# Kernel optimization log

Hardware: AMD Instinct MI355X
Metric: run time of the kernel (lower is better)

## Reference

```python
import jax, jax.numpy as jnp
import numpy as np

# Model dims
D_MODEL = 768
N_LAYER = 2
VOCAB = 32000
D_STATE = 16
D_INNER = 2 * D_MODEL          # expand=2
DT_RANK = D_MODEL // 16        # 48
D_CONV = 4
EPS = 1e-5


def rmsnorm(x, w):
    return x * jax.lax.rsqrt(jnp.mean(x * x, axis=-1, keepdims=True) + EPS) * w


def selective_scan(u, delta, A, B, C, D):
    # u: (b,l,di) delta: (b,l,di) A: (di,n) B,C: (b,l,n) D: (di,)
    def step(h, inp):
        delta_t, B_t, C_t, u_t = inp  # (b,di),(b,n),(b,n),(b,di)
        dA = jnp.exp(delta_t[..., None] * A)                      # (b,di,n)
        dBu = delta_t[..., None] * B_t[:, None, :] * u_t[..., None]
        h = dA * h + dBu
        y = jnp.einsum('bdn,bn->bd', h, C_t)
        return h, y

    b = u.shape[0]
    h0 = jnp.zeros((b, D_INNER, D_STATE), dtype=u.dtype)
    xs = (jnp.swapaxes(delta, 0, 1), jnp.swapaxes(B, 0, 1),
          jnp.swapaxes(C, 0, 1), jnp.swapaxes(u, 0, 1))
    _, ys = jax.lax.scan(step, h0, xs)        # ys: (l,b,di)
    y = jnp.swapaxes(ys, 0, 1)
    return y + u * D


def mamba_block(x, in_proj_w, conv_w, conv_b, x_proj_w, dt_proj_w, dt_proj_b,
                A_log, D, out_proj_w):
    b, l, d = x.shape
    xr = x @ in_proj_w.T                       # (b,l,2*di)
    u, res = jnp.split(xr, 2, axis=-1)
    # causal depthwise conv over seq
    uc = jnp.swapaxes(u, 1, 2)                 # (b,di,l)
    uc = jax.lax.conv_general_dilated(
        uc, conv_w[:, None, :], window_strides=(1,),
        padding=[(D_CONV - 1, 0)], feature_group_count=D_INNER,
        dimension_numbers=('NCH', 'OIH', 'NCH'))
    u = jax.nn.silu(jnp.swapaxes(uc + conv_b[None, :, None], 1, 2))
    # ssm
    A = -jnp.exp(A_log)                        # (di,n)
    x_dbl = u @ x_proj_w.T                     # (b,l,dt_rank+2n)
    delta, B, C = jnp.split(x_dbl, [DT_RANK, DT_RANK + D_STATE], axis=-1)
    delta = jax.nn.softplus(delta @ dt_proj_w.T + dt_proj_b)   # (b,l,di)
    y = selective_scan(u, delta, A, B, C, D)
    y = y * jax.nn.silu(res)
    return y @ out_proj_w.T


def setup_inputs() -> dict:
    key = jax.random.key(0)
    ks = jax.random.split(key, 12)
    s = 0.02
    L = N_LAYER
    inp = {
        'input_ids': jax.random.randint(ks[0], (2, 1024), 0, VOCAB),
        'emb': jax.random.normal(ks[1], (VOCAB, D_MODEL), jnp.float32) * s,
        'norm_w': jnp.ones((L, D_MODEL), jnp.float32),
        'in_proj_w': jax.random.normal(ks[2], (L, 2 * D_INNER, D_MODEL), jnp.float32) * s,
        'conv_w': jax.random.normal(ks[3], (L, D_INNER, D_CONV), jnp.float32) * s,
        'conv_b': jnp.zeros((L, D_INNER), jnp.float32),
        'x_proj_w': jax.random.normal(ks[4], (L, DT_RANK + 2 * D_STATE, D_INNER), jnp.float32) * s,
        'dt_proj_w': jax.random.normal(ks[5], (L, D_INNER, DT_RANK), jnp.float32) * s,
        'dt_proj_b': jax.random.normal(ks[6], (L, D_INNER), jnp.float32) * s,
        'A_log': jnp.log(jnp.broadcast_to(jnp.arange(1, D_STATE + 1, dtype=jnp.float32),
                                          (L, D_INNER, D_STATE))),
        'D': jnp.ones((L, D_INNER), jnp.float32),
        'out_proj_w': jax.random.normal(ks[7], (L, D_MODEL, D_INNER), jnp.float32) * s,
        'norm_f_w': jnp.ones((D_MODEL,), jnp.float32),
    }
    return inp


def reference(input_ids, emb, norm_w, in_proj_w, conv_w, conv_b, x_proj_w,
              dt_proj_w, dt_proj_b, A_log, D, out_proj_w, norm_f_w):
    x = emb[input_ids]                         # (b,l,d)
    for i in range(N_LAYER):
        x = x + mamba_block(rmsnorm(x, norm_w[i]), in_proj_w[i], conv_w[i],
                            conv_b[i], x_proj_w[i], dt_proj_w[i], dt_proj_b[i],
                            A_log[i], D[i], out_proj_w[i])
    x = rmsnorm(x, norm_f_w)
    logits = x @ emb.T                         # tied lm_head
    return logits
```

## Files before the change

kernel.cpp:

```cpp
#include <hip/hip_runtime.h>
#include <hip/hip_bf16.h>
#include <cstdint>
#include <cstddef>

#define D_MODEL 768
#define D_INNER 1536
#define DT_RANK 48
#define D_STATE 16
#define SEQ     1024
#define BATCH   2
#define NROWS   2048
#define VOCAB   32000
#define LCHUNK  16
#define NCHUNK  64
#define CHST    49152

typedef __hip_bfloat16 bf16;
typedef short bf16x8 __attribute__((ext_vector_type(8)));
typedef float f32x4  __attribute__((ext_vector_type(4)));
struct bf8 { bf16 v[8]; };

__device__ __forceinline__ void async_copy16(void* lds, const void* gp) {
    __builtin_amdgcn_global_load_lds(
        (const __attribute__((address_space(1))) unsigned int*)gp,
        (__attribute__((address_space(3)))       unsigned int*)lds,
        16, 0, 0);
}

template<int EPI>
__global__ __launch_bounds__(256) void gemm_bt(
    const bf16* __restrict__ A, const bf16* __restrict__ B,
    float* __restrict__ C, const float* __restrict__ bias,
    int M, int N, int K, int ntm)
{
    __shared__ bf16 sA[128 * 32];
    __shared__ bf16 sB[128 * 32];
    const int bid  = blockIdx.x;
    const int m0   = (bid % ntm) * 128;
    const int n0   = (bid / ntm) * 128;
    const int t    = threadIdx.x;
    const int wave = t >> 6;
    const int lane = t & 63;
    const int r0 = wave * 16 + (lane >> 2);
    const int c0 = (lane & 3) * 8;
    const int wm = (wave & 1) * 64;
    const int wn = (wave >> 1) * 64;
    const int fm = lane & 15;
    const int kq = (lane >> 4) * 8;

    f32x4 acc[4][4];
    #pragma unroll
    for (int i = 0; i < 4; ++i)
        #pragma unroll
        for (int j = 0; j < 4; ++j)
            acc[i][j] = {0.f, 0.f, 0.f, 0.f};

    int nr0 = n0 + r0;      if (nr0 > N - 1) nr0 = N - 1;
    int nr1 = n0 + 64 + r0; if (nr1 > N - 1) nr1 = N - 1;

    const bf16* gA0 = A + (size_t)(m0 + r0)      * K + c0;
    const bf16* gA1 = A + (size_t)(m0 + 64 + r0) * K + c0;
    const bf16* gB0 = B + (size_t)nr0 * K + c0;
    const bf16* gB1 = B + (size_t)nr1 * K + c0;
    char* lA0 = (char*)sA + wave * 1024;
    char* lA1 = (char*)sA + 4096 + wave * 1024;
    char* lB0 = (char*)sB + wave * 1024;
    char* lB1 = (char*)sB + 4096 + wave * 1024;

    for (int k0 = 0; k0 < K; k0 += 32) {
        async_copy16(lA0, gA0 + k0);
        async_copy16(lA1, gA1 + k0);
        async_copy16(lB0, gB0 + k0);
        async_copy16(lB1, gB1 + k0);
        __syncthreads();

        bf16x8 af[4], bfr[4];
        #pragma unroll
        for (int i = 0; i < 4; ++i) {
            af[i]  = *(const bf16x8*)&sA[(wm + i * 16 + fm) * 32 + kq];
            bfr[i] = *(const bf16x8*)&sB[(wn + i * 16 + fm) * 32 + kq];
        }
        #pragma unroll
        for (int i = 0; i < 4; ++i)
            #pragma unroll
            for (int j = 0; j < 4; ++j)
                acc[i][j] = __builtin_amdgcn_mfma_f32_16x16x32_bf16(
                    af[i], bfr[j], acc[i][j], 0, 0, 0);
        __syncthreads();
    }

    const int lr = (lane >> 4) * 4;
    const int lc = lane & 15;
    #pragma unroll
    for (int i = 0; i < 4; ++i) {
        #pragma unroll
        for (int j = 0; j < 4; ++j) {
            const int col = n0 + wn + j * 16 + lc;
            if (col >= N) continue;
            #pragma unroll
            for (int r = 0; r < 4; ++r) {
                const int row = m0 + wm + i * 16 + lr + r;
                const size_t o = (size_t)row * N + col;
                float v = acc[i][j][r];
                if (EPI == 1) {
                    C[o] += v;
                } else if (EPI == 2) {
                    v += bias[col];
                    v = (v > 15.f) ? v : __logf(1.f + __expf(v));
                    C[o] = v;
                } else {
                    C[o] = v;
                }
            }
        }
    }
}

__global__ __launch_bounds__(192) void embed_kernel(
    const int* __restrict__ ids, const float* __restrict__ emb,
    float* __restrict__ x)
{
    const int row = blockIdx.x;
    const int t = threadIdx.x;
    const float4* src = (const float4*)(emb + (size_t)ids[row] * D_MODEL);
    float4* dst = (float4*)(x + (size_t)row * D_MODEL);
    dst[t] = src[t];
}

__global__ __launch_bounds__(256) void rmsnorm_kernel(
    const float* __restrict__ x, const float* __restrict__ w,
    bf16* __restrict__ out)
{
    const int row = blockIdx.x;
    const float* xr = x + (size_t)row * D_MODEL;
    const int t = threadIdx.x;
    float v0 = xr[t], v1 = xr[t + 256], v2 = xr[t + 512];
    float s = v0 * v0 + v1 * v1 + v2 * v2;
    #pragma unroll
    for (int m = 1; m < 64; m <<= 1) s += __shfl_xor(s, m);
    __shared__ float red[4];
    if ((t & 63) == 0) red[t >> 6] = s;
    __syncthreads();
    s = red[0] + red[1] + red[2] + red[3];
    const float sc = rsqrtf(s * (1.f / 768.f) + 1e-5f);
    bf16* o = out + (size_t)row * D_MODEL;
    o[t]       = __float2bfloat16(v0 * sc * w[t]);
    o[t + 256] = __float2bfloat16(v1 * sc * w[t + 256]);
    o[t + 512] = __float2bfloat16(v2 * sc * w[t + 512]);
}

__global__ __launch_bounds__(256) void cvt_bf16_kernel(
    const float* __restrict__ src, bf16* __restrict__ dst, int n)
{
    const int i = (blockIdx.x * 256 + threadIdx.x) * 8;
    if (i >= n) return;
    const float4 a = *(const float4*)(src + i);
    const float4 b = *(const float4*)(src + i + 4);
    bf8 o;
    o.v[0] = __float2bfloat16(a.x); o.v[1] = __float2bfloat16(a.y);
    o.v[2] = __float2bfloat16(a.z); o.v[3] = __float2bfloat16(a.w);
    o.v[4] = __float2bfloat16(b.x); o.v[5] = __float2bfloat16(b.y);
    o.v[6] = __float2bfloat16(b.z); o.v[7] = __float2bfloat16(b.w);
    *(bf8*)(dst + i) = o;
}

__global__ __launch_bounds__(256) void cvt_layer_weights(
    const float* __restrict__ ipw, const float* __restrict__ xpw,
    const float* __restrict__ dtw, const float* __restrict__ opw,
    bf16* __restrict__ wip, bf16* __restrict__ wxp,
    bf16* __restrict__ wdt, bf16* __restrict__ wop)
{
    int i = blockIdx.x * 256 + threadIdx.x;
    if (i < 3072 * 768) { wip[i] = __float2bfloat16(ipw[i]); return; }
    i -= 3072 * 768;
    if (i < 80 * 1536)  { wxp[i] = __float2bfloat16(xpw[i]); return; }
    i -= 80 * 1536;
    if (i < 1536 * 64) {
        const int r = i >> 6, c = i & 63;
        wdt[i] = __float2bfloat16(c < DT_RANK ? dtw[r * DT_RANK + c] : 0.f);
        return;
    }
    i -= 1536 * 64;
    if (i < 768 * 1536) { wop[i] = __float2bfloat16(opw[i]); }
}

__global__ __launch_bounds__(256) void pad_dt_kernel(
    const float* __restrict__ x_dbl, bf16* __restrict__ out)
{
    const int i = blockIdx.x * 256 + threadIdx.x;
    const int r = i >> 6, c = i & 63;
    out[i] = __float2bfloat16(c < DT_RANK ? x_dbl[r * 80 + c] : 0.f);
}

__global__ __launch_bounds__(256) void conv_silu_kernel(
    const float* __restrict__ xr, const float* __restrict__ cw,
    const float* __restrict__ cb, float* __restrict__ uf,
    bf16* __restrict__ ub)
{
    const int idx = blockIdx.x * 256 + threadIdx.x;
    const int di  = idx % D_INNER;
    const int row = idx / D_INNER;
    const int l   = row & (SEQ - 1);
    float acc = cb[di];
    #pragma unroll
    for (int j = 0; j < 4; ++j) {
        const int ll = l - 3 + j;
        if (ll >= 0)
            acc += cw[di * 4 + j] * xr[(size_t)(row - 3 + j) * 3072 + di];
    }
    const float s = acc / (1.f + __expf(-acc));
    uf[idx] = s;
    ub[idx] = __float2bfloat16(s);
}

__global__ __launch_bounds__(256) void scan_pass1(
    const float* __restrict__ delta, const float* __restrict__ u,
    const float* __restrict__ x_dbl, const float* __restrict__ A_log,
    float* __restrict__ P, float* __restrict__ H)
{
    const int n  = threadIdx.x & 15;
    const int g  = threadIdx.x >> 4;
    const int ch = blockIdx.x * 16 + g;
    const int k  = blockIdx.y;
    const int b  = ch / D_INNER;
    const int di = ch % D_INNER;
    const int t0 = k * LCHUNK;

    const float An = -__expf(A_log[di * D_STATE + n]);
    const float* drow = delta + ((size_t)b * SEQ + t0) * D_INNER + di;
    const float* urow = u     + ((size_t)b * SEQ + t0) * D_INNER + di;
    const float* xdr  = x_dbl + ((size_t)b * SEQ + t0) * 80;

    float h = 0.f, ap = 1.f;
    #pragma unroll
    for (int t = 0; t < LCHUNK; ++t) {
        const float dv = drow[t * D_INNER];
        const float uv = urow[t * D_INNER];
        const float Bv = xdr[t * 80 + 48 + n];
        const float a  = __expf(dv * An);
        h = a * h + (dv * Bv) * uv;
        ap *= a;
    }
    const size_t o = (size_t)k * CHST + ch * 16 + n;
    P[o] = ap;
    H[o] = h;
}

__global__ __launch_bounds__(256) void scan_pass2(
    const float* __restrict__ P, const float* __restrict__ H,
    float* __restrict__ Hin)
{
    const int id = blockIdx.x * 256 + threadIdx.x;
    float h = 0.f;
    #pragma unroll 16
    for (int k = 0; k < NCHUNK; ++k) {
        const size_t o = (size_t)k * CHST + id;
        Hin[o] = h;
        h = P[o] * h + H[o];
    }
}

__global__ __launch_bounds__(256) void scan_pass3(
    const float* __restrict__ delta, const float* __restrict__ u,
    const float* __restrict__ x_dbl, const float* __restrict__ xr,
    const float* __restrict__ A_log, const float* __restrict__ Dp,
    const float* __restrict__ Hin, bf16* __restrict__ yb)
{
    const int n  = threadIdx.x & 15;
    const int g  = threadIdx.x >> 4;
    const int ch = blockIdx.x * 16 + g;
    const int k  = blockIdx.y;
    const int b  = ch / D_INNER;
    const int di = ch % D_INNER;
    const int t0 = k * LCHUNK;

    const float An = -__expf(A_log[di * D_STATE + n]);
    const float Dv = Dp[di];
    const float* drow = delta + ((size_t)b * SEQ + t0) * D_INNER + di;
    const float* urow = u     + ((size_t)b * SEQ + t0) * D_INNER + di;
    const float* rrow = xr + ((size_t)b * SEQ + t0) * 3072 + D_INNER + di;
    const float* xdr  = x_dbl + ((size_t)b * SEQ + t0) * 80;
    bf16* yrow = yb + ((size_t)b * SEQ + t0) * D_INNER + di;

    float h = Hin[(size_t)k * CHST + ch * 16 + n];
    #pragma unroll
    for (int t = 0; t < LCHUNK; ++t) {
        const float dv = drow[t * D_INNER];
        const float uv = urow[t * D_INNER];
        const float Bv = xdr[t * 80 + 48 + n];
        const float Cv = xdr[t * 80 + 64 + n];
        const float a  = __expf(dv * An);
        h = a * h + (dv * Bv) * uv;
        float p = h * Cv;
        p += __shfl_xor(p, 1);
        p += __shfl_xor(p, 2);
        p += __shfl_xor(p, 4);
        p += __shfl_xor(p, 8);
        if (n == 0) {
            float y = p + uv * Dv;
            const float r = rrow[t * 3072];
            y *= r / (1.f + __expf(-r));
            yrow[t * D_INNER] = __float2bfloat16(y);
        }
    }
}

extern "C" void kernel_launch(void* const* d_in, const int* in_sizes, int n_in,
                              void* d_out, int out_size, void* d_ws, size_t ws_size,
                              hipStream_t stream)
{
    const int*   ids    = (const int*)  d_in[0];
    const float* emb    = (const float*)d_in[1];
    const float* norm_w = (const float*)d_in[2];
    const float* ipw    = (const float*)d_in[3];
    const float* cw     = (const float*)d_in[4];
    const float* cb     = (const float*)d_in[5];
    const float* xpw    = (const float*)d_in[6];
    const float* dtw    = (const float*)d_in[7];
    const float* dtb    = (const float*)d_in[8];
    const float* alog   = (const float*)d_in[9];
    const float* Dp     = (const float*)d_in[10];
    const float* opw    = (const float*)d_in[11];
    const float* nfw    = (const float*)d_in[12];
    float* out = (float*)d_out;

    char* ws = (char*)d_ws;
    bf16*  emb_bf = (bf16*)ws;  ws += (size_t)VOCAB * D_MODEL * 2;
    float* x      = (float*)ws; ws += (size_t)NROWS * D_MODEL * 4;
    bf16*  xn     = (bf16*)ws;  ws += (size_t)NROWS * D_MODEL * 2;
    bf16*  ub     = (bf16*)ws;  ws += (size_t)NROWS * D_INNER * 2;
    float* xdbl   = (float*)ws; ws += (size_t)NROWS * 80 * 4;
    bf16*  dtraw  = (bf16*)ws;  ws += (size_t)NROWS * 64 * 2;
    bf16*  yb     = (bf16*)ws;  ws += (size_t)NROWS * D_INNER * 2;
    bf16*  wip    = (bf16*)ws;  ws += (size_t)3072 * 768 * 2;
    bf16*  wxp    = (bf16*)ws;  ws += (size_t)80 * 1536 * 2;
    bf16*  wdt    = (bf16*)ws;  ws += (size_t)1536 * 64 * 2;
    bf16*  wop    = (bf16*)ws;  ws += (size_t)768 * 1536 * 2;

    char* ob = (char*)d_out;
    float* xr    = (float*)ob;  ob += (size_t)NROWS * 3072 * 4;
    float* uf    = (float*)ob;  ob += (size_t)NROWS * D_INNER * 4;
    float* delta = (float*)ob;  ob += (size_t)NROWS * D_INNER * 4;
    float* Pbuf  = (float*)ob;  ob += (size_t)NCHUNK * CHST * 4;
    float* Hbuf  = (float*)ob;  ob += (size_t)NCHUNK * CHST * 4;
    float* Hin   = (float*)ob;  ob += (size_t)NCHUNK * CHST * 4;

    cvt_bf16_kernel<<<VOCAB * D_MODEL / 8 / 256, 256, 0, stream>>>(
        emb, emb_bf, VOCAB * D_MODEL);
    embed_kernel<<<NROWS, 192, 0, stream>>>(ids, emb, x);

    for (int l = 0; l < 2; ++l) {
        cvt_layer_weights<<<(3760128 + 255) / 256, 256, 0, stream>>>(
            ipw + (size_t)l * 3072 * 768, xpw + (size_t)l * 80 * 1536,
            dtw + (size_t)l * 1536 * DT_RANK, opw + (size_t)l * 768 * 1536,
            wip, wxp, wdt, wop);
        rmsnorm_kernel<<<NROWS, 256, 0, stream>>>(x, norm_w + l * D_MODEL, xn);
        gemm_bt<0><<<16 * 24, 256, 0, stream>>>(xn, wip, xr, nullptr,
                                                NROWS, 3072, D_MODEL, 16);
        conv_silu_kernel<<<NROWS * D_INNER / 256, 256, 0, stream>>>(
            xr, cw + (size_t)l * D_INNER * 4, cb + (size_t)l * D_INNER, uf, ub);
        gemm_bt<0><<<16 * 1, 256, 0, stream>>>(ub, wxp, xdbl, nullptr,
                                               NROWS, 80, D_INNER, 16);
        pad_dt_kernel<<<NROWS * 64 / 256, 256, 0, stream>>>(xdbl, dtraw);
        gemm_bt<2><<<16 * 12, 256, 0, stream>>>(dtraw, wdt, delta,
                                                dtb + (size_t)l * D_INNER,
                                                NROWS, D_INNER, 64, 16);
        scan_pass1<<<dim3(192, NCHUNK), 256, 0, stream>>>(
            delta, uf, xdbl, alog + (size_t)l * D_INNER * D_STATE, Pbuf, Hbuf);
        scan_pass2<<<CHST / 256, 256, 0, stream>>>(Pbuf, Hbuf, Hin);
        scan_pass3<<<dim3(192, NCHUNK), 256, 0, stream>>>(
            delta, uf, xdbl, xr, alog + (size_t)l * D_INNER * D_STATE,
            Dp + (size_t)l * D_INNER, Hin, yb);
        gemm_bt<1><<<16 * 6, 256, 0, stream>>>(yb, wop, x, nullptr,
                                               NROWS, D_MODEL, D_INNER, 16);
    }

    rmsnorm_kernel<<<NROWS, 256, 0, stream>>>(x, nfw, xn);
    gemm_bt<0><<<16 * 250, 256, 0, stream>>>(xn, emb_bf, out, nullptr,
                                             NROWS, VOCAB, D_MODEL, 16);
}
```

Measured before the change: 1.054 ms.

## Add 256x256 pipelined GEMM for lm_head and split-K the x_proj GEMM

Adds a 512-thread GEMM kernel with 256x256 tiles, 64-wide K steps, double-buffered swizzled LDS staging via async global-to-LDS loads, interleaved MFMA phases and an XCD-aware block remap. It is used for the large tied lm_head projection (2048x32000x768), which dominates runtime. The tiny x_proj GEMM, previously launched on only 16 blocks, is split along K into 4 partial products and then reduced by a new kernel to raise parallelism. The new kernel uses 128KB of LDS and relies on the dimensions dividing 256 exactly, with no bounds checks.

```diff
diff --git a/kernel.cpp b/kernel.cpp
--- a/kernel.cpp
+++ b/kernel.cpp
@@ -27,17 +27,165 @@
         16, 0, 0);
 }
 
+
+#define LDSP(BUF, AB) (smem + (((BUF)*2 + (AB)) << 15))
+
+#define PHB() do { \
+  __builtin_amdgcn_sched_barrier(0); \
+  __builtin_amdgcn_s_barrier(); \
+  __builtin_amdgcn_sched_barrier(0); \
+} while (0)
+
+#define WAIT_VMCNT(n) do { \
+  asm volatile("s_waitcnt vmcnt(" #n ")" ::: "memory"); \
+  __builtin_amdgcn_sched_barrier(0); \
+} while (0)
+
+#define STAGE_A(BUF, H, KT) do { \
+  const int ru0_ = (H)*64 + wave*8; \
+  const int ru1_ = ru0_ + 128; \
+  const bf16* ga0_ = Ag + (size_t)(m0 + ru0_ + (lane >> 3)) * (size_t)K + (size_t)((KT)*64 + swz8); \
+  const bf16* ga1_ = Ag + (size_t)(m0 + ru1_ + (lane >> 3)) * (size_t)K + (size_t)((KT)*64 + swz8); \
+  async_copy16(LDSP(BUF, 0) + ru0_*128, ga0_); \
+  async_copy16(LDSP(BUF, 0) + ru1_*128, ga1_); \
+} while (0)
+
+#define STAGE_B(BUF, H, KT) do { \
+  const int lb0_ = wave*8, lb1_ = 64 + wave*8; \
+  const int rb0_ = ((lb0_ >> 5) << 6) + (H)*32 + (lb0_ & 31); \
+  const int rb1_ = ((lb1_ >> 5) << 6) + (H)*32 + (lb1_ & 31); \
+  const bf16* gb0_ = Bg + (size_t)(n0 + rb0_ + (lane >> 3)) * (size_t)K + (size_t)((KT)*64 + swz8); \
+  const bf16* gb1_ = Bg + (size_t)(n0 + rb1_ + (lane >> 3)) * (size_t)K + (size_t)((KT)*64 + swz8); \
+  async_copy16(LDSP(BUF, 1) + rb0_*128, gb0_); \
+  async_copy16(LDSP(BUF, 1) + rb1_*128, gb1_); \
+} while (0)
+
+#define RDA4(BUF, MH) do { \
+  _Pragma("unroll") \
+  for (int i2_ = 0; i2_ < 4; ++i2_) { \
+    const char* rp_ = LDSP(BUF, 0) + (wr*128 + (MH)*64 + i2_*16 + fm) * 128; \
+    a[i2_][0] = *(const bf16x8*)(rp_ + (((kqi    ) ^ fm7) << 4)); \
+    a[i2_][1] = *(const bf16x8*)(rp_ + (((4 + kqi) ^ fm7) << 4)); \
+  } \
+} while (0)
+
+#define RDB4(BUF, NH, DST) do { \
+  _Pragma("unroll") \
+  for (int j2_ = 0; j2_ < 2; ++j2_) { \
+    const char* rp_ = LDSP(BUF, 1) + (wc*64 + (NH)*32 + j2_*16 + fm) * 128; \
+    DST[j2_][0] = *(const bf16x8*)(rp_ + (((kqi    ) ^ fm7) << 4)); \
+    DST[j2_][1] = *(const bf16x8*)(rp_ + (((4 + kqi) ^ fm7) << 4)); \
+  } \
+} while (0)
+
+#define QMFMA(MH, NH, BB) do { \
+  __builtin_amdgcn_s_setprio(1); \
+  _Pragma("unroll") \
+  for (int i2_ = 0; i2_ < 4; ++i2_) { \
+    _Pragma("unroll") \
+    for (int j2_ = 0; j2_ < 2; ++j2_) { \
+      acc[(MH)*4 + i2_][(NH)*2 + j2_] = __builtin_amdgcn_mfma_f32_16x16x32_bf16( \
+          a[i2_][0], BB[j2_][0], acc[(MH)*4 + i2_][(NH)*2 + j2_], 0, 0, 0); \
+      acc[(MH)*4 + i2_][(NH)*2 + j2_] = __builtin_amdgcn_mfma_f32_16x16x32_bf16( \
+          a[i2_][1], BB[j2_][1], acc[(MH)*4 + i2_][(NH)*2 + j2_], 0, 0, 0); \
+    } \
+  } \
+  __builtin_amdgcn_s_setprio(0); \
+} while (0)
+
+#define ITER(TT, LAST) do { \
+  RDA4(0, 0); RDB4(0, 0, b0); \
+  STAGE_B(1, 1, (TT) + 1); \
+  PHB(); QMFMA(0, 0, b0); PHB(); \
+  RDB4(0, 1, b1); \
+  if (!(LAST)) STAGE_A(0, 0, (TT) + 2); \
+  PHB(); QMFMA(0, 1, b1); PHB(); \
+  RDA4(0, 1); \
+  if (!(LAST)) STAGE_B(0, 0, (TT) + 2); \
+  PHB(); QMFMA(1, 0, b0); PHB(); \
+  if (!(LAST)) { STAGE_A(0, 1, (TT) + 2); WAIT_VMCNT(6); } else { WAIT_VMCNT(0); } \
+  PHB(); QMFMA(1, 1, b1); PHB(); \
+  RDA4(1, 0); RDB4(1, 0, b0); \
+  if (!(LAST)) STAGE_B(0, 1, (TT) + 2); \
+  PHB(); QMFMA(0, 0, b0); PHB(); \
+  RDB4(1, 1, b1); \
+  if (!(LAST)) STAGE_A(1, 0, (TT) + 3); \
+  PHB(); QMFMA(0, 1, b1); PHB(); \
+  RDA4(1, 1); \
+  if (!(LAST)) STAGE_B(1, 0, (TT) + 3); \
+  PHB(); QMFMA(1, 0, b0); PHB(); \
+  if (!(LAST)) { STAGE_A(1, 1, (TT) + 3); WAIT_VMCNT(6); } else { WAIT_VMCNT(0); } \
+  PHB(); QMFMA(1, 1, b1); PHB(); \
+} while (0)
+
+__global__ __launch_bounds__(512, 2) void gemm256(
+    const bf16* __restrict__ Ag, const bf16* __restrict__ Bg,
+    float* __restrict__ C, int M, int N, int K, int ntm)
+{
+    (void)M;
+    __shared__ __align__(16) char smem[131072];
+
+    const int cpx  = gridDim.x >> 3;
+    const int bid  = blockIdx.x;
+    const int wgid = (bid & 7) * cpx + (bid >> 3);
+    const int m0 = (wgid % ntm) << 8;
+    const int n0 = (wgid / ntm) << 8;
+
+    const int t    = threadIdx.x;
+    const int wave = t >> 6, lane = t & 63;
+    const int wr = wave >> 2, wc = wave & 3;
+    const int fm  = lane & 15, fm7 = lane & 7;
+    const int kqi = lane >> 4;
+    const int swz8 = (((lane & 7) ^ ((lane >> 3) & 7)) << 3);
+    const int nkt = K >> 6;
+
+    f32x4 acc[8][4];
+    #pragma unroll
+    for (int i = 0; i < 8; ++i)
+        #pragma unroll
+        for (int j = 0; j < 4; ++j)
+            acc[i][j] = {0.f, 0.f, 0.f, 0.f};
+
+    bf16x8 a[4][2], b0[2][2], b1[2][2];
+
+    STAGE_A(0, 0, 0); STAGE_A(0, 1, 0); STAGE_B(0, 0, 0); STAGE_B(0, 1, 0);
+    WAIT_VMCNT(4);
+    STAGE_A(1, 0, 1); STAGE_A(1, 1, 1); STAGE_B(1, 0, 1);
+    WAIT_VMCNT(6);
+    PHB();
+
+    int tt = 0;
+    #pragma unroll 1
+    for (; tt + 2 < nkt; tt += 2) { ITER(tt, false); }
+    ITER(tt, true);
+
+    const int lr = (lane >> 4) * 4;
+    const int lc = lane & 15;
+    #pragma unroll
+    for (int i = 0; i < 8; ++i) {
+        #pragma unroll
+        for (int j = 0; j < 4; ++j) {
+            const size_t base = (size_t)(m0 + wr*128 + i*16 + lr) * N
+                              + (size_t)(n0 + wc*64 + j*16 + lc);
+            #pragma unroll
+            for (int r = 0; r < 4; ++r)
+                C[base + (size_t)r * N] = acc[i][j][r];
+        }
+    }
+}
+
 template<int EPI>
 __global__ __launch_bounds__(256) void gemm_bt(
     const bf16* __restrict__ A, const bf16* __restrict__ B,
     float* __restrict__ C, const float* __restrict__ bias,
-    int M, int N, int K, int ntm)
+    int M, int N, int K, int lda, int ntm)
 {
     __shared__ bf16 sA[128 * 32];
     __shared__ bf16 sB[128 * 32];
     const int bid  = blockIdx.x;
     const int m0   = (bid % ntm) * 128;
     const int n0   = (bid / ntm) * 128;
+    const int koff = blockIdx.y * K;
     const int t    = threadIdx.x;
     const int wave = t >> 6;
     const int lane = t & 63;
@@ -58,14 +206,16 @@
     int nr0 = n0 + r0;      if (nr0 > N - 1) nr0 = N - 1;
     int nr1 = n0 + 64 + r0; if (nr1 > N - 1) nr1 = N - 1;
 
-    const bf16* gA0 = A + (size_t)(m0 + r0)      * K + c0;
-    const bf16* gA1 = A + (size_t)(m0 + 64 + r0) * K + c0;
-    const bf16* gB0 = B + (size_t)nr0 * K + c0;
-    const bf16* gB1 = B + (size_t)nr1 * K + c0;
+    const bf16* gA0 = A + (size_t)(m0 + r0)      * lda + koff + c0;
+    const bf16* gA1 = A + (size_t)(m0 + 64 + r0) * lda + koff + c0;
+    const bf16* gB0 = B + (size_t)nr0 * lda + koff + c0;
+    const bf16* gB1 = B + (size_t)nr1 * lda + koff + c0;
     char* lA0 = (char*)sA + wave * 1024;
     char* lA1 = (char*)sA + 4096 + wave * 1024;
     char* lB0 = (char*)sB + wave * 1024;
     char* lB1 = (char*)sB + 4096 + wave * 1024;
+
+    C += (size_t)blockIdx.y * M * N;
 
     for (int k0 = 0; k0 < K; k0 += 32) {
         async_copy16(lA0, gA0 + k0);
@@ -116,6 +266,14 @@
     }
 }
 
+__global__ __launch_bounds__(256) void reduce4_kernel(
+    const float* __restrict__ p, float* __restrict__ o, int n)
+{
+    const int i = blockIdx.x * 256 + threadIdx.x;
+    if (i >= n) return;
+    o[i] = p[i] + p[i + n] + p[i + 2 * n] + p[i + 3 * n];
+}
+
 __global__ __launch_bounds__(192) void embed_kernel(
     const int* __restrict__ ids, const float* __restrict__ emb,
     float* __restrict__ x)
@@ -344,6 +502,7 @@
     float* Pbuf  = (float*)ob;  ob += (size_t)NCHUNK * CHST * 4;
     float* Hbuf  = (float*)ob;  ob += (size_t)NCHUNK * CHST * 4;
     float* Hin   = (float*)ob;  ob += (size_t)NCHUNK * CHST * 4;
+    float* xpart = (float*)ob;  ob += (size_t)4 * NROWS * 80 * 4;
 
     cvt_bf16_kernel<<<VOCAB * D_MODEL / 8 / 256, 256, 0, stream>>>(
         emb, emb_bf, VOCAB * D_MODEL);
@@ -356,15 +515,17 @@
             wip, wxp, wdt, wop);
         rmsnorm_kernel<<<NROWS, 256, 0, stream>>>(x, norm_w + l * D_MODEL, xn);
         gemm_bt<0><<<16 * 24, 256, 0, stream>>>(xn, wip, xr, nullptr,
-                                                NROWS, 3072, D_MODEL, 16);
+                                                NROWS, 3072, D_MODEL, D_MODEL, 16);
         conv_silu_kernel<<<NROWS * D_INNER / 256, 256, 0, stream>>>(
             xr, cw + (size_t)l * D_INNER * 4, cb + (size_t)l * D_INNER, uf, ub);
-        gemm_bt<0><<<16 * 1, 256, 0, stream>>>(ub, wxp, xdbl, nullptr,
-                                               NROWS, 80, D_INNER, 16);
+        gemm_bt<0><<<dim3(16, 4), 256, 0, stream>>>(ub, wxp, xpart, nullptr,
+                                                    NROWS, 80, 384, D_INNER, 16);
+        reduce4_kernel<<<(NROWS * 80 + 255) / 256, 256, 0, stream>>>(
+            xpart, xdbl, NROWS * 80);
         pad_dt_kernel<<<NROWS * 64 / 256, 256, 0, stream>>>(xdbl, dtraw);
         gemm_bt<2><<<16 * 12, 256, 0, stream>>>(dtraw, wdt, delta,
                                                 dtb + (size_t)l * D_INNER,
-                                                NROWS, D_INNER, 64, 16);
+                                                NROWS, D_INNER, 64, 64, 16);
         scan_pass1<<<dim3(192, NCHUNK), 256, 0, stream>>>(
             delta, uf, xdbl, alog + (size_t)l * D_INNER * D_STATE, Pbuf, Hbuf);
         scan_pass2<<<CHST / 256, 256, 0, stream>>>(Pbuf, Hbuf, Hin);
@@ -372,10 +533,10 @@
             delta, uf, xdbl, xr, alog + (size_t)l * D_INNER * D_STATE,
             Dp + (size_t)l * D_INNER, Hin, yb);
         gemm_bt<1><<<16 * 6, 256, 0, stream>>>(yb, wop, x, nullptr,
-                                               NROWS, D_MODEL, D_INNER, 16);
+                                               NROWS, D_MODEL, D_INNER, D_INNER, 16);
     }
 
     rmsnorm_kernel<<<NROWS, 256, 0, stream>>>(x, nfw, xn);
-    gemm_bt<0><<<16 * 250, 256, 0, stream>>>(xn, emb_bf, out, nullptr,
-                                             NROWS, VOCAB, D_MODEL, 16);
-}
+    gemm256<<<8 * 125, 512, 0, stream>>>(xn, emb_bf, out,
+                                         NROWS, VOCAB, D_MODEL, 8);
+}
```

After: 971.4 us. 1.08x faster.
